# Kernel optimization log

Hardware: AMD Instinct MI355X
Metric: run time of the kernel (lower is better)

## Reference

```python
import jax, jax.numpy as jnp
import numpy as np

N, P, H = 4096, 128, 4
E = P // H           # per-head embed dim (=32)
NSEG = 32            # number of distinct position segments
NEG = -1e30          # mask fill (safe finite -inf)


def setup_inputs() -> dict:
    key = jax.random.key(0)
    ks = jax.random.split(key, 8)
    s = 1.0 / np.sqrt(P)
    return {
        "inp": jax.random.normal(ks[0], (N, P), jnp.float32),
        "pos": jax.random.randint(ks[1], (N,), 0, NSEG, jnp.int32),
        "Wq": jax.random.normal(ks[2], (P, P), jnp.float32) * s,
        "bq": jnp.zeros((P,), jnp.float32),
        "Wk": jax.random.normal(ks[3], (P, P), jnp.float32) * s,
        "bk": jnp.zeros((P,), jnp.float32),
        "Wv": jax.random.normal(ks[4], (P, P), jnp.float32) * s,
        "bv": jnp.zeros((P,), jnp.float32),
    }


def reference(inp, pos, Wq, bq, Wk, bk, Wv, bv):
    # Per-segment multi-head self-attention. The TF while_loop gathers rows of
    # each unique `pos` value, runs attention within that segment, and scatters
    # results back to the original row order. This is mathematically identical
    # to full attention with a same-segment mask (softmax restricted to keys
    # in the same segment), which is the vectorized form here.
    n = inp.shape[0]

    def heads(x, W, b):
        # (n, p) -> (h, n, e), matching rearrange 'n (h e) -> h n e'
        y = x @ W + b
        return y.reshape(n, H, E).transpose(1, 0, 2)

    q = heads(inp, Wq, bq)
    k = heads(inp, Wk, bk)
    v = heads(inp, Wv, bv)

    score = jnp.einsum('hne,hme->hnm', q, k) / np.sqrt(E).astype(np.float32)
    same_seg = (pos[:, None] == pos[None, :])[None, :, :]      # (1, n, n)
    score = jnp.where(same_seg, score, NEG)
    weight = jax.nn.softmax(score, axis=-1)                    # (h, n, n)
    out = jnp.einsum('hnm,hme->hne', weight, v)                # (h, n, e)
    # rearrange 'h n e -> n (h e)'
    return out.transpose(1, 0, 2).reshape(n, P)
```

## Files before the change

kernel.cpp:

```cpp
#include <hip/hip_runtime.h>
#include <hip/hip_bf16.h>
#include <math.h>

#define N 4096
#define P 128
#define H 4
#define E 32
#define NSEG 32
#define TPB 256
#define PROJ_TASKS 192

#define VSTRIDE 264
#define NEGF -3.0e38f

typedef __attribute__((ext_vector_type(8))) short bf16x8;
typedef __attribute__((ext_vector_type(4))) float f32x4;
typedef unsigned short u16;

__device__ __forceinline__ u16 f2b(float x) {
    __hip_bfloat16 b = __float2bfloat16(x);
    return *(u16*)&b;
}

__device__ __forceinline__ void sort_phase(const int* __restrict__ pos,
                                           int* __restrict__ seg_rows,
                                           int* __restrict__ seg_off,
                                           int* sm, int t) {
    int* cnt = sm;
    int* cur = sm + NSEG;
    int* off = sm + 2 * NSEG;
    if (t < NSEG) cnt[t] = 0;
    __syncthreads();
    for (int i = t; i < N; i += TPB) atomicAdd(&cnt[pos[i]], 1);
    __syncthreads();
    if (t == 0) {
        int s = 0;
        for (int k = 0; k < NSEG; ++k) { off[k] = s; s += cnt[k]; }
        off[NSEG] = s;
    }
    __syncthreads();
    if (t <= NSEG) seg_off[t] = off[t];
    if (t < NSEG) cur[t] = off[t];
    __syncthreads();
    for (int i = t; i < N; i += TPB) {
        int r = atomicAdd(&cur[pos[i]], 1);
        seg_rows[r] = i;
    }
}

__device__ __forceinline__ void proj_phase(int task,
                                           const float* __restrict__ x,
                                           const float* __restrict__ Wq, const float* __restrict__ bq,
                                           const float* __restrict__ Wk, const float* __restrict__ bk,
                                           const float* __restrict__ Wv, const float* __restrict__ bv,
                                           u16* __restrict__ Q, u16* __restrict__ Ko, u16* __restrict__ Vo,
                                           float* sm, int t) {
    float* Xl = sm;
    float* Wl = sm + 8192;

    const int mat = task >> 6;
    const int r0  = (task & 63) * 64;
    const float* W = (mat == 0) ? Wq : (mat == 1) ? Wk : Wv;
    const float* b = (mat == 0) ? bq : (mat == 1) ? bk : bv;
    u16* y         = (mat == 0) ? Q  : (mat == 1) ? Ko : Vo;

    for (int i = t * 4; i < 64 * 128; i += TPB * 4) {
        *(float4*)(Xl + i) = *(const float4*)(x + (size_t)r0 * 128 + i);
    }

    const int tc = t & 31;
    const int tr = t >> 5;

    float4 bb = *(const float4*)(b + tc * 4);
    float4 acc[8];
#pragma unroll
    for (int r = 0; r < 8; ++r) acc[r] = bb;

    for (int kc = 0; kc < 128; kc += 32) {
        __syncthreads();
        for (int i = t * 4; i < 32 * 128; i += TPB * 4) {
            *(float4*)(Wl + i) = *(const float4*)(W + (size_t)kc * 128 + i);
        }
        __syncthreads();
#pragma unroll
        for (int k0 = 0; k0 < 32; k0 += 4) {
            float4 w0 = *(float4*)&Wl[(k0 + 0) * 128 + tc * 4];
            float4 w1 = *(float4*)&Wl[(k0 + 1) * 128 + tc * 4];
            float4 w2 = *(float4*)&Wl[(k0 + 2) * 128 + tc * 4];
            float4 w3 = *(float4*)&Wl[(k0 + 3) * 128 + tc * 4];
#pragma unroll
            for (int r = 0; r < 8; ++r) {
                float4 xv = *(float4*)&Xl[(tr * 8 + r) * 128 + kc + k0];
                acc[r].x = fmaf(xv.x, w0.x, acc[r].x);
                acc[r].y = fmaf(xv.x, w0.y, acc[r].y);
                acc[r].z = fmaf(xv.x, w0.z, acc[r].z);
                acc[r].w = fmaf(xv.x, w0.w, acc[r].w);
                acc[r].x = fmaf(xv.y, w1.x, acc[r].x);
                acc[r].y = fmaf(xv.y, w1.y, acc[r].y);
                acc[r].z = fmaf(xv.y, w1.z, acc[r].z);
                acc[r].w = fmaf(xv.y, w1.w, acc[r].w);
                acc[r].x = fmaf(xv.z, w2.x, acc[r].x);
                acc[r].y = fmaf(xv.z, w2.y, acc[r].y);
                acc[r].z = fmaf(xv.z, w2.z, acc[r].z);
                acc[r].w = fmaf(xv.z, w2.w, acc[r].w);
                acc[r].x = fmaf(xv.w, w3.x, acc[r].x);
                acc[r].y = fmaf(xv.w, w3.y, acc[r].y);
                acc[r].z = fmaf(xv.w, w3.z, acc[r].z);
                acc[r].w = fmaf(xv.w, w3.w, acc[r].w);
            }
        }
    }

#pragma unroll
    for (int r = 0; r < 8; ++r) {
        ushort4 st;
        st.x = f2b(acc[r].x); st.y = f2b(acc[r].y);
        st.z = f2b(acc[r].z); st.w = f2b(acc[r].w);
        *(ushort4*)(y + (size_t)(r0 + tr * 8 + r) * 128 + tc * 4) = st;
    }
}

__global__ __launch_bounds__(TPB) void sort_proj_kernel(
        const float* __restrict__ inp, const int* __restrict__ pos,
        const float* __restrict__ Wq, const float* __restrict__ bq,
        const float* __restrict__ Wk, const float* __restrict__ bk,
        const float* __restrict__ Wv, const float* __restrict__ bv,
        u16* __restrict__ Q, u16* __restrict__ Kb, u16* __restrict__ Vb,
        int* __restrict__ seg_rows, int* __restrict__ seg_off) {
    __shared__ __align__(16) float sm[12288];
    const int b = blockIdx.x;
    const int t = threadIdx.x;
    if (b == 0) {
        sort_phase(pos, seg_rows, seg_off, (int*)sm, t);
    } else {
        proj_phase(b - 1, inp, Wq, bq, Wk, bk, Wv, bv, Q, Kb, Vb, sm, t);
    }
}

template <int KT>
__device__ __forceinline__ void attn_body(int beg, int len, int h, int z,
                                          const u16* __restrict__ Qb,
                                          const u16* __restrict__ Kb,
                                          const u16* __restrict__ Vb,
                                          const int* __restrict__ seg_rows,
                                          float* __restrict__ out,
                                          u16* __restrict__ smu,
                                          int t, int w, int col, int quad) {
    const float scale = 0.17677669529663687f;
    u16* Vt = smu;
    u16* Ps = smu + (32 + w * 16) * VSTRIDE;

#pragma unroll
    for (int ii = 0; ii < KT / 4; ++ii) {
        const int idx = ii * TPB + t;
        const int key = idx >> 2, c = idx & 3;
        bf16x8 v = {0, 0, 0, 0, 0, 0, 0, 0};
        if (key < len)
            v = *(const bf16x8*)(Vb + (size_t)seg_rows[beg + key] * 128 + h * 32 + c * 8);
#pragma unroll
        for (int j = 0; j < 8; ++j)
            Vt[(c * 8 + j) * VSTRIDE + key] = (u16)v[j];
    }

    const int tt = z * 4 + w;
    const bool have = (tt * 16 < len);
    float lrow[4];

    if (have) {
        const int qi = beg + min(tt * 16 + col, len - 1);
        const bf16x8 qa = *(const bf16x8*)(Qb + (size_t)seg_rows[qi] * 128 + h * 32 + quad * 8);

        int krow[KT];
#pragma unroll
        for (int kt = 0; kt < KT; ++kt)
            krow[kt] = seg_rows[beg + min(kt * 16 + col, len - 1)];

        f32x4 S[KT];
#pragma unroll
        for (int kt = 0; kt < KT; ++kt) {
            const bf16x8 kb = *(const bf16x8*)(Kb + (size_t)krow[kt] * 128 + h * 32 + quad * 8);
            f32x4 c = {0.f, 0.f, 0.f, 0.f};
            S[kt] = __builtin_amdgcn_mfma_f32_16x16x32_bf16(qa, kb, c, 0, 0, 0);
        }

        float mrow[4] = {NEGF, NEGF, NEGF, NEGF};
#pragma unroll
        for (int kt = 0; kt < KT; ++kt) {
            const bool kvalid = (kt * 16 + col) < len;
#pragma unroll
            for (int r = 0; r < 4; ++r) {
                const float sc = kvalid ? S[kt][r] * scale : NEGF;
                S[kt][r] = sc;
                mrow[r] = fmaxf(mrow[r], sc);
            }
        }
#pragma unroll
        for (int d = 1; d < 16; d <<= 1) {
#pragma unroll
            for (int r = 0; r < 4; ++r)
                mrow[r] = fmaxf(mrow[r], __shfl_xor(mrow[r], d));
        }
        lrow[0] = lrow[1] = lrow[2] = lrow[3] = 0.f;
#pragma unroll
        for (int kt = 0; kt < KT; ++kt) {
#pragma unroll
            for (int r = 0; r < 4; ++r) {
                const float p = __expf(S[kt][r] - mrow[r]);
                S[kt][r] = p;
                lrow[r] += p;
            }
        }
#pragma unroll
        for (int d = 1; d < 16; d <<= 1) {
#pragma unroll
            for (int r = 0; r < 4; ++r)
                lrow[r] += __shfl_xor(lrow[r], d);
        }
#pragma unroll
        for (int kt = 0; kt < KT; ++kt) {
#pragma unroll
            for (int r = 0; r < 4; ++r)
                Ps[(quad * 4 + r) * VSTRIDE + kt * 16 + col] = f2b(S[kt][r]);
        }
    }

    __syncthreads();

    if (have) {
        f32x4 o0 = {0.f, 0.f, 0.f, 0.f}, o1 = {0.f, 0.f, 0.f, 0.f};
#pragma unroll
        for (int kg = 0; kg < KT / 2; ++kg) {
            const bf16x8 pa = *(const bf16x8*)(Ps + col * VSTRIDE + kg * 32 + quad * 8);
            const bf16x8 v0 = *(const bf16x8*)(Vt + col * VSTRIDE + kg * 32 + quad * 8);
            const bf16x8 v1 = *(const bf16x8*)(Vt + (16 + col) * VSTRIDE + kg * 32 + quad * 8);
            o0 = __builtin_amdgcn_mfma_f32_16x16x32_bf16(pa, v0, o0, 0, 0, 0);
            o1 = __builtin_amdgcn_mfma_f32_16x16x32_bf16(pa, v1, o1, 0, 0, 0);
        }
#pragma unroll
        for (int r = 0; r < 4; ++r) {
            const int qloc = tt * 16 + quad * 4 + r;
            if (qloc < len) {
                const int orow = seg_rows[beg + qloc];
                const float inv = 1.0f / lrow[r];
                float* op = out + (size_t)orow * 128 + h * 32;
                op[col]      = o0[r] * inv;
                op[16 + col] = o1[r] * inv;
            }
        }
    }
}

__global__ __launch_bounds__(TPB) void attn_kernel(const u16* __restrict__ Qb,
                                                   const u16* __restrict__ Kb,
                                                   const u16* __restrict__ Vb,
                                                   const int* __restrict__ seg_rows,
                                                   const int* __restrict__ seg_off,
                                                   float* __restrict__ out) {
    __shared__ u16 smu[VSTRIDE * (32 + 4 * 16)];

    const int s = blockIdx.x, h = blockIdx.y, z = blockIdx.z;
    const int beg = seg_off[s];
    const int len = seg_off[s + 1] - beg;
    if (z * 64 >= len) return;
    const int t = threadIdx.x, w = t >> 6;
    const int lane = t & 63, col = lane & 15, quad = lane >> 4;

    if (len <= 128)
        attn_body<8>(beg, len, h, z, Qb, Kb, Vb, seg_rows, out, smu, t, w, col, quad);
    else
        attn_body<16>(beg, len, h, z, Qb, Kb, Vb, seg_rows, out, smu, t, w, col, quad);
}

extern "C" void kernel_launch(void* const* d_in, const int* in_sizes, int n_in,
                              void* d_out, int out_size, void* d_ws, size_t ws_size,
                              hipStream_t stream) {
    const float* inp = (const float*)d_in[0];
    const int*   pos = (const int*)d_in[1];
    const float* Wq  = (const float*)d_in[2];
    const float* bq  = (const float*)d_in[3];
    const float* Wk  = (const float*)d_in[4];
    const float* bk  = (const float*)d_in[5];
    const float* Wv  = (const float*)d_in[6];
    const float* bv  = (const float*)d_in[7];
    float* out = (float*)d_out;

    u16* Qb = (u16*)d_ws;
    u16* Kb = Qb + (size_t)N * 128;
    u16* Vb = Kb + (size_t)N * 128;
    int* seg_rows = (int*)(Vb + (size_t)N * 128);
    int* seg_off  = seg_rows + N;

    sort_proj_kernel<<<1 + PROJ_TASKS, TPB, 0, stream>>>(
        inp, pos, Wq, bq, Wk, bk, Wv, bv, Qb, Kb, Vb, seg_rows, seg_off);

    attn_kernel<<<dim3(NSEG, H, 4), TPB, 0, stream>>>(
        Qb, Kb, Vb, seg_rows, seg_off, out);
}
```

Baseline: 92.02 us.

## Use split-bf16 MFMA for QKV projection and per-wave counters in segment sort

The fp32 FMA projection, which staged tiles through 48KB of LDS, becomes bf16 MFMA 16x16x32 ops. Each fp32 operand is split into hi and lo bf16 parts and combined with three MFMAs to keep near-fp32 accuracy, with operands read straight from global memory. The sort phase now uses per-wave histogram counters and a warp-shuffle scan, which cuts atomic contention and the serial single-thread prefix sum. In exchange, weight loads are strided and uncoalesced (column gathers), stores are scalar, and LDS use falls sharply, which may allow higher occupancy.

```diff
diff --git a/kernel.cpp b/kernel.cpp
--- a/kernel.cpp
+++ b/kernel.cpp
@@ -22,28 +22,47 @@
     return *(u16*)&b;
 }
 
+__device__ __forceinline__ void split_tr(float v, short& hi, short& lo) {
+    unsigned bits = __float_as_uint(v);
+    unsigned hbits = bits & 0xFFFF0000u;
+    float r = v - __uint_as_float(hbits);
+    hi = (short)(bits >> 16);
+    lo = (short)(__float_as_uint(r) >> 16);
+}
+
 __device__ __forceinline__ void sort_phase(const int* __restrict__ pos,
                                            int* __restrict__ seg_rows,
                                            int* __restrict__ seg_off,
                                            int* sm, int t) {
     int* cnt = sm;
-    int* cur = sm + NSEG;
-    int* off = sm + 2 * NSEG;
-    if (t < NSEG) cnt[t] = 0;
+    int* off = sm + 128;
+    int* cur = sm + 161;
+    const int w = t >> 6;
+    if (t < 128) cnt[t] = 0;
     __syncthreads();
-    for (int i = t; i < N; i += TPB) atomicAdd(&cnt[pos[i]], 1);
+    for (int i = t; i < N; i += TPB) atomicAdd(&cnt[(w << 5) + pos[i]], 1);
     __syncthreads();
-    if (t == 0) {
-        int s = 0;
-        for (int k = 0; k < NSEG; ++k) { off[k] = s; s += cnt[k]; }
-        off[NSEG] = s;
+    if (t < 32) {
+        const int c0 = cnt[t], c1 = cnt[32 + t], c2 = cnt[64 + t], c3 = cnt[96 + t];
+        const int tot = c0 + c1 + c2 + c3;
+        int x = tot;
+#pragma unroll
+        for (int d = 1; d < 32; d <<= 1) {
+            int y = __shfl_up(x, d);
+            if (t >= d) x += y;
+        }
+        const int excl = x - tot;
+        off[t] = excl;
+        if (t == 31) off[32] = x;
+        cur[t]      = excl;
+        cur[32 + t] = excl + c0;
+        cur[64 + t] = excl + c0 + c1;
+        cur[96 + t] = excl + c0 + c1 + c2;
     }
     __syncthreads();
     if (t <= NSEG) seg_off[t] = off[t];
-    if (t < NSEG) cur[t] = off[t];
-    __syncthreads();
     for (int i = t; i < N; i += TPB) {
-        int r = atomicAdd(&cur[pos[i]], 1);
+        const int r = atomicAdd(&cur[(w << 5) + pos[i]], 1);
         seg_rows[r] = i;
     }
 }
@@ -54,69 +73,58 @@
                                            const float* __restrict__ Wk, const float* __restrict__ bk,
                                            const float* __restrict__ Wv, const float* __restrict__ bv,
                                            u16* __restrict__ Q, u16* __restrict__ Ko, u16* __restrict__ Vo,
-                                           float* sm, int t) {
-    float* Xl = sm;
-    float* Wl = sm + 8192;
-
+                                           int t) {
     const int mat = task >> 6;
     const int r0  = (task & 63) * 64;
     const float* W = (mat == 0) ? Wq : (mat == 1) ? Wk : Wv;
     const float* b = (mat == 0) ? bq : (mat == 1) ? bk : bv;
     u16* y         = (mat == 0) ? Q  : (mat == 1) ? Ko : Vo;
 
-    for (int i = t * 4; i < 64 * 128; i += TPB * 4) {
-        *(float4*)(Xl + i) = *(const float4*)(x + (size_t)r0 * 128 + i);
-    }
-
-    const int tc = t & 31;
-    const int tr = t >> 5;
-
-    float4 bb = *(const float4*)(b + tc * 4);
-    float4 acc[8];
-#pragma unroll
-    for (int r = 0; r < 8; ++r) acc[r] = bb;
-
-    for (int kc = 0; kc < 128; kc += 32) {
-        __syncthreads();
-        for (int i = t * 4; i < 32 * 128; i += TPB * 4) {
-            *(float4*)(Wl + i) = *(const float4*)(W + (size_t)kc * 128 + i);
-        }
-        __syncthreads();
-#pragma unroll
-        for (int k0 = 0; k0 < 32; k0 += 4) {
-            float4 w0 = *(float4*)&Wl[(k0 + 0) * 128 + tc * 4];
-            float4 w1 = *(float4*)&Wl[(k0 + 1) * 128 + tc * 4];
-            float4 w2 = *(float4*)&Wl[(k0 + 2) * 128 + tc * 4];
-            float4 w3 = *(float4*)&Wl[(k0 + 3) * 128 + tc * 4];
-#pragma unroll
-            for (int r = 0; r < 8; ++r) {
-                float4 xv = *(float4*)&Xl[(tr * 8 + r) * 128 + kc + k0];
-                acc[r].x = fmaf(xv.x, w0.x, acc[r].x);
-                acc[r].y = fmaf(xv.x, w0.y, acc[r].y);
-                acc[r].z = fmaf(xv.x, w0.z, acc[r].z);
-                acc[r].w = fmaf(xv.x, w0.w, acc[r].w);
-                acc[r].x = fmaf(xv.y, w1.x, acc[r].x);
-                acc[r].y = fmaf(xv.y, w1.y, acc[r].y);
-                acc[r].z = fmaf(xv.y, w1.z, acc[r].z);
-                acc[r].w = fmaf(xv.y, w1.w, acc[r].w);
-                acc[r].x = fmaf(xv.z, w2.x, acc[r].x);
-                acc[r].y = fmaf(xv.z, w2.y, acc[r].y);
-                acc[r].z = fmaf(xv.z, w2.z, acc[r].z);
-                acc[r].w = fmaf(xv.z, w2.w, acc[r].w);
-                acc[r].x = fmaf(xv.w, w3.x, acc[r].x);
-                acc[r].y = fmaf(xv.w, w3.y, acc[r].y);
-                acc[r].z = fmaf(xv.w, w3.z, acc[r].z);
-                acc[r].w = fmaf(xv.w, w3.w, acc[r].w);
+    const int w = t >> 6, lane = t & 63, col = lane & 15, quad = lane >> 4;
+    const int arow = r0 + w * 16 + col;
+
+    f32x4 acc[8];
+#pragma unroll
+    for (int cf = 0; cf < 8; ++cf) {
+        const float bb = b[cf * 16 + col];
+        acc[cf] = (f32x4){bb, bb, bb, bb};
+    }
+
+#pragma unroll
+    for (int kc = 0; kc < 4; ++kc) {
+        const float* xp = x + (size_t)arow * 128 + kc * 32 + quad * 8;
+        const float4 a0 = *(const float4*)xp;
+        const float4 a1 = *(const float4*)(xp + 4);
+        const float af[8] = {a0.x, a0.y, a0.z, a0.w, a1.x, a1.y, a1.z, a1.w};
+        bf16x8 ah, al;
+#pragma unroll
+        for (int j = 0; j < 8; ++j) {
+            short h, l; split_tr(af[j], h, l);
+            ah[j] = h; al[j] = l;
+        }
+
+        const float* wp = W + (size_t)(kc * 32 + quad * 8) * 128 + col;
+#pragma unroll
+        for (int cf = 0; cf < 8; ++cf) {
+            const float* wc = wp + cf * 16;
+            bf16x8 bh, bl;
+#pragma unroll
+            for (int j = 0; j < 8; ++j) {
+                short h, l; split_tr(wc[j * 128], h, l);
+                bh[j] = h; bl[j] = l;
             }
-        }
-    }
-
-#pragma unroll
-    for (int r = 0; r < 8; ++r) {
-        ushort4 st;
-        st.x = f2b(acc[r].x); st.y = f2b(acc[r].y);
-        st.z = f2b(acc[r].z); st.w = f2b(acc[r].w);
-        *(ushort4*)(y + (size_t)(r0 + tr * 8 + r) * 128 + tc * 4) = st;
+            acc[cf] = __builtin_amdgcn_mfma_f32_16x16x32_bf16(ah, bh, acc[cf], 0, 0, 0);
+            acc[cf] = __builtin_amdgcn_mfma_f32_16x16x32_bf16(al, bh, acc[cf], 0, 0, 0);
+            acc[cf] = __builtin_amdgcn_mfma_f32_16x16x32_bf16(ah, bl, acc[cf], 0, 0, 0);
+        }
+    }
+
+#pragma unroll
+    for (int cf = 0; cf < 8; ++cf) {
+#pragma unroll
+        for (int r = 0; r < 4; ++r) {
+            y[(size_t)(r0 + w * 16 + quad * 4 + r) * 128 + cf * 16 + col] = f2b(acc[cf][r]);
+        }
     }
 }
 
@@ -127,13 +135,13 @@
         const float* __restrict__ Wv, const float* __restrict__ bv,
         u16* __restrict__ Q, u16* __restrict__ Kb, u16* __restrict__ Vb,
         int* __restrict__ seg_rows, int* __restrict__ seg_off) {
-    __shared__ __align__(16) float sm[12288];
+    __shared__ int smi[292];
     const int b = blockIdx.x;
     const int t = threadIdx.x;
     if (b == 0) {
-        sort_phase(pos, seg_rows, seg_off, (int*)sm, t);
+        sort_phase(pos, seg_rows, seg_off, smi, t);
     } else {
-        proj_phase(b - 1, inp, Wq, bq, Wk, bk, Wv, bv, Q, Kb, Vb, sm, t);
+        proj_phase(b - 1, inp, Wq, bq, Wk, bk, Wv, bv, Q, Kb, Vb, t);
     }
 }
 
```

Measured after the change: 84.79 us. -7.9%, faster.
